# Optimization experiments

Measured on AMD Instinct MI355X. Metric: run time of the kernel, lower is better.

## Reference

```python
import jax, jax.numpy as jnp
import numpy as np


def setup_inputs() -> dict:
    key = jax.random.key(0)
    k1, k2, k3, k4 = jax.random.split(key, 4)
    B, S, D = 8, 2048, 512
    scale = 1.0 / np.sqrt(D)
    return {
        "x": jax.random.normal(k1, (B, S, D), dtype=jnp.float32),
        "WQ": jax.random.normal(k2, (D, D), dtype=jnp.float32) * scale,
        "WK": jax.random.normal(k3, (D, D), dtype=jnp.float32) * scale,
        "WV": jax.random.normal(k4, (D, D), dtype=jnp.float32) * scale,
    }


def reference(x, WQ, WK, WV):
    # x: [B, S, D]; single-head scaled dot-product self-attention
    Q = jnp.einsum("bsd,de->bse", x, WQ)
    K = jnp.einsum("bsd,de->bse", x, WK)
    V = jnp.einsum("bsd,de->bse", x, WV)
    d_k = jnp.asarray(K.shape[-1], dtype=x.dtype)
    scores = jnp.einsum("bqd,bkd->bqk", Q, K) / jnp.sqrt(d_k)  # [B,S,S]
    weights = jax.nn.softmax(scores, axis=-1)
    return jnp.einsum("bqk,bkd->bqd", weights, V)
```

## Files before the change

kernel.cpp:

```cpp
#include <hip/hip_runtime.h>
#include <cstdint>
#include <cstddef>

#define B_ 8
#define S_ 2048
#define D_ 512

typedef float f32x4 __attribute__((ext_vector_type(4)));
typedef __bf16 bf16x8 __attribute__((ext_vector_type(8)));

__device__ __forceinline__ unsigned short f2bf(float f) {
    unsigned u = __builtin_bit_cast(unsigned, f);
    u += 0x7FFFu + ((u >> 16) & 1u);
    return (unsigned short)(u >> 16);
}

template<int MT>
__global__ __launch_bounds__(256, (MT == 8) ? 2 : 3) void gemm_bt(
    const unsigned short* __restrict__ A,
    const unsigned short* __restrict__ B,
    void* __restrict__ Cv,
    unsigned short* __restrict__ Cv2,
    float* __restrict__ rs_part,
    int K, int lda, int ldb, int ldc,
    long long sA, long long sB, long long sC,
    float scale, int mode, int ntn, int nbatch)
{
    constexpr int TM = MT * 32;
    __shared__ __align__(16) unsigned short lA[TM * 32];
    __shared__ __align__(16) unsigned short lB[128 * 32];

    const int lin = blockIdx.x;
    const int bz  = lin % nbatch;
    const int t   = lin / nbatch;
    const int tn  = t % ntn;
    const int tm  = t / ntn;

    A += (long long)bz * sA;
    B += (long long)bz * sB;
    const int m0 = tm * TM;
    const int n0 = tn * 128;
    const int tid  = threadIdx.x;
    const int lane = tid & 63;
    const int wave = tid >> 6;
    const int wm = (wave & 1) * (MT * 16);
    const int wn = (wave >> 1) * 64;

    f32x4 acc[MT][4] = {};

    const int abase = wave * (MT * 512);
    const unsigned short* Ap[MT / 2];
    int aoff[MT / 2];
    #pragma unroll
    for (int j = 0; j < MT / 2; ++j) {
        const int o = abase + j * 1024 + lane * 16;
        aoff[j] = o;
        const int r = o >> 6, cp = (o & 63) >> 4;
        const int c = (cp ^ ((r >> 1) & 3)) << 3;
        Ap[j] = A + (size_t)(m0 + r) * lda + c;
    }
    const int bo0 = wave * 2048, bo1 = bo0 + 1024;
    const int ob0 = bo0 + lane * 16, ob1 = bo1 + lane * 16;
    const int rB0 = ob0 >> 6, cB0 = ((((ob0 & 63) >> 4) ^ ((rB0 >> 1) & 3)) << 3);
    const int rB1 = ob1 >> 6, cB1 = ((((ob1 & 63) >> 4) ^ ((rB1 >> 1) & 3)) << 3);
    const unsigned short* B0 = B + (size_t)(n0 + rB0) * ldb + cB0;
    const unsigned short* B1 = B + (size_t)(n0 + rB1) * ldb + cB1;

    char* lAc = (char*)lA;
    char* lBc = (char*)lB;

    const int fr  = lane & 15;
    const int g   = lane >> 4;
    const int sx  = (g ^ ((fr >> 1) & 3)) << 3;

    bf16x8 sa[MT / 2], sb0, sb1;
    #pragma unroll
    for (int j = 0; j < MT / 2; ++j)
        sa[j] = *(const bf16x8*)(Ap[j]);
    sb0 = *(const bf16x8*)(B0);
    sb1 = *(const bf16x8*)(B1);

    for (int k0 = 0; k0 < K; k0 += 32) {
        __syncthreads();
        #pragma unroll
        for (int j = 0; j < MT / 2; ++j)
            *(bf16x8*)(lAc + aoff[j]) = sa[j];
        *(bf16x8*)(lBc + ob0) = sb0;
        *(bf16x8*)(lBc + ob1) = sb1;
        __syncthreads();

        if (k0 + 32 < K) {
            #pragma unroll
            for (int j = 0; j < MT / 2; ++j)
                sa[j] = *(const bf16x8*)(Ap[j] + k0 + 32);
            sb0 = *(const bf16x8*)(B0 + k0 + 32);
            sb1 = *(const bf16x8*)(B1 + k0 + 32);
        }

        bf16x8 af[MT], bfv[4];
        #pragma unroll
        for (int mt = 0; mt < MT; ++mt)
            af[mt] = *(const bf16x8*)&lA[(wm + mt * 16 + fr) * 32 + sx];
        #pragma unroll
        for (int nt = 0; nt < 4; ++nt)
            bfv[nt] = *(const bf16x8*)&lB[(wn + nt * 16 + fr) * 32 + sx];
        #pragma unroll
        for (int mt = 0; mt < MT; ++mt)
            #pragma unroll
            for (int nt = 0; nt < 4; ++nt)
                acc[mt][nt] = __builtin_amdgcn_mfma_f32_16x16x32_bf16(
                    af[mt], bfv[nt], acc[mt][nt], 0, 0, 0);
    }

    const int rb = g << 2;

    if (mode == 1) {
        #pragma unroll
        for (int mt = 0; mt < MT; ++mt)
            #pragma unroll
            for (int nt = 0; nt < 4; ++nt)
                #pragma unroll
                for (int r = 0; r < 4; ++r)
                    acc[mt][nt][r] = __expf(acc[mt][nt][r] * scale);

        unsigned short* C = (unsigned short*)Cv + (long long)bz * sC;
        #pragma unroll
        for (int mt = 0; mt < MT; ++mt)
            #pragma unroll
            for (int nt = 0; nt < 4; ++nt) {
                const int gc = n0 + wn + nt * 16 + fr;
                #pragma unroll
                for (int r = 0; r < 4; ++r)
                    C[(size_t)(m0 + wm + mt * 16 + rb + r) * ldc + gc] =
                        f2bf(acc[mt][nt][r]);
            }

        float* rp = rs_part + (((long long)bz * S_) << 5) + tn * 2 + (wn >> 6);
        #pragma unroll
        for (int mt = 0; mt < MT; ++mt)
            #pragma unroll
            for (int r = 0; r < 4; ++r) {
                float s = acc[mt][0][r] + acc[mt][1][r] +
                          acc[mt][2][r] + acc[mt][3][r];
                s += __shfl_xor(s, 8);
                s += __shfl_xor(s, 4);
                s += __shfl_xor(s, 2);
                s += __shfl_xor(s, 1);
                if (fr == 0)
                    rp[(long long)(m0 + wm + mt * 16 + rb + r) << 5] = s;
            }
    } else if (mode == 3) {
        if (tn >= 8) {
            #pragma unroll
            for (int mt = 0; mt < MT; ++mt) {
                const int s0q = m0 + wm + mt * 16 + rb;
                const int b   = s0q >> 11;
                const int se  = s0q & (S_ - 1);
                #pragma unroll
                for (int nt = 0; nt < 4; ++nt) {
                    const int d = (n0 - 1024) + wn + nt * 16 + fr;
                    ushort4 u;
                    u.x = f2bf(acc[mt][nt][0]);
                    u.y = f2bf(acc[mt][nt][1]);
                    u.z = f2bf(acc[mt][nt][2]);
                    u.w = f2bf(acc[mt][nt][3]);
                    *(ushort4*)&Cv2[((size_t)b * D_ + d) * S_ + se] = u;
                }
            }
        } else {
            unsigned short* C = (unsigned short*)Cv;
            #pragma unroll
            for (int mt = 0; mt < MT; ++mt)
                #pragma unroll
                for (int nt = 0; nt < 4; ++nt) {
                    const int gc = n0 + wn + nt * 16 + fr;
                    #pragma unroll
                    for (int r = 0; r < 4; ++r)
                        C[(size_t)(m0 + wm + mt * 16 + rb + r) * ldc + gc] =
                            f2bf(acc[mt][nt][r]);
                }
        }
    } else {
        float* C = (float*)Cv + (long long)bz * sC;
        #pragma unroll
        for (int nt = 0; nt < 4; ++nt) {
            const int q = n0 + wn + nt * 16 + fr;
            const float* rp = rs_part + (((long long)bz * S_ + q) << 5);
            float ssum = 0.f;
            #pragma unroll
            for (int pq = 0; pq < 8; ++pq) {
                const float4 p4 = *(const float4*)(rp + 4 * pq);
                ssum += (p4.x + p4.y) + (p4.z + p4.w);
            }
            const float inv = __builtin_amdgcn_rcpf(ssum);
            #pragma unroll
            for (int mt = 0; mt < MT; ++mt) {
                const int d0 = m0 + wm + mt * 16 + rb;
                float4 o;
                o.x = acc[mt][nt][0] * inv;
                o.y = acc[mt][nt][1] * inv;
                o.z = acc[mt][nt][2] * inv;
                o.w = acc[mt][nt][3] * inv;
                *(float4*)&C[(size_t)q * ldc + d0] = o;
            }
        }
    }
}

__global__ __launch_bounds__(256) void convert_x4(const float* __restrict__ x,
                                                  unsigned short* __restrict__ xb) {
    const size_t i = ((size_t)blockIdx.x * 256 + threadIdx.x) * 4;
    const float4 f = *(const float4*)(x + i);
    ushort4 u;
    u.x = f2bf(f.x); u.y = f2bf(f.y); u.z = f2bf(f.z); u.w = f2bf(f.w);
    *(ushort4*)(xb + i) = u;
}

__global__ __launch_bounds__(256) void convert_w(const float* __restrict__ WQ,
                                                 const float* __restrict__ WK,
                                                 const float* __restrict__ WV,
                                                 unsigned short* __restrict__ WT) {
    const int o = blockIdx.x * 256 + threadIdx.x;
    const float* W = blockIdx.y == 0 ? WQ : (blockIdx.y == 1 ? WK : WV);
    const int e = o >> 9, d = o & (D_ - 1);
    WT[(size_t)blockIdx.y * D_ * D_ + o] = f2bf(W[d * D_ + e]);
}

extern "C" void kernel_launch(void* const* d_in, const int* in_sizes, int n_in,
                              void* d_out, int out_size, void* d_ws, size_t ws_size,
                              hipStream_t stream)
{
    const float* x  = (const float*)d_in[0];
    const float* WQ = (const float*)d_in[1];
    const float* WK = (const float*)d_in[2];
    const float* WV = (const float*)d_in[3];

    unsigned short* ws  = (unsigned short*)d_ws;
    const size_t NX = (size_t)B_ * S_ * D_;
    unsigned short* xb  = ws;
    unsigned short* wtb = xb + NX;
    unsigned short* qk  = wtb + 3 * D_ * D_;
    unsigned short* vtb = qk + NX * 2;
    unsigned short* sb  = vtb + NX;
    float* rsp = (float*)(sb + (size_t)B_ * S_ * S_);

    convert_x4<<<dim3((unsigned)(NX / 4 / 256)), 256, 0, stream>>>(x, xb);
    convert_w<<<dim3(D_ * D_ / 256, 3), 256, 0, stream>>>(WQ, WK, WV, wtb);

    gemm_bt<8><<<dim3((B_ * S_ / 256) * (3 * D_ / 128)), 256, 0, stream>>>(
        xb, wtb, qk, vtb, nullptr, D_, D_, D_, 2 * D_,
        0, 0, 0, 1.0f, 3,  3 * D_ / 128,  1);

    gemm_bt<8><<<dim3(B_ * (S_ / 256) * (S_ / 128)), 256, 0, stream>>>(
        qk , qk + D_ , sb, nullptr, rsp, D_, 2 * D_, 2 * D_, S_,
        (long long)S_ * 2 * D_, (long long)S_ * 2 * D_, (long long)S_ * S_,
        0.04419417382415922f, 1,  S_ / 128,  B_);

    gemm_bt<4><<<dim3(B_ * (D_ / 128) * (S_ / 128)), 256, 0, stream>>>(
        vtb, sb, d_out, nullptr, rsp, S_, S_, S_, D_,
        (long long)D_ * S_, (long long)S_ * S_, (long long)S_ * D_,
        1.0f, 0,  S_ / 128,  B_);
}
```

Baseline: 235.7 us.

## Rewrite GEMM as 8-wave 256x256 tile with direct global-to-LDS async double buffering

Replaces the 4-wave register-staged GEMM with an 8-wave kernel using 256x256 (or 128x256) tiles, K-step 64, and global_load_lds to stream tiles straight into a double-buffered swizzled LDS. The main loop is split into four phases, each with explicit vmcnt waits and barriers, so half-tile loads overlap MFMA work, and s_setprio raises priority during the MFMA bursts. The goal is to cut LDS staging through registers, raise arithmetic intensity and hide memory latency. Larger tiles give fewer blocks per GEMM, which risks lower occupancy and tail imbalance. The hand-counted vmcnt values are fragile.

```diff
diff --git a/kernel.cpp b/kernel.cpp
--- a/kernel.cpp
+++ b/kernel.cpp
@@ -15,8 +15,18 @@
     return (unsigned short)(u >> 16);
 }
 
-template<int MT>
-__global__ __launch_bounds__(256, (MT == 8) ? 2 : 3) void gemm_bt(
+__device__ __forceinline__ void gll16(const void* g, void* l) {
+    __builtin_amdgcn_global_load_lds(
+        (const __attribute__((address_space(1))) unsigned int*)g,
+        (__attribute__((address_space(3))) unsigned int*)l, 16, 0, 0);
+}
+
+#define VMCNT(n) asm volatile("s_waitcnt vmcnt(%0)" :: "i"(n) : "memory")
+#define PHASE_FENCE() do { asm volatile("" ::: "memory"); \
+                           __builtin_amdgcn_sched_barrier(0); } while (0)
+
+template<int AMT, int BNT>
+__global__ __launch_bounds__(512, 2) void gemm8(
     const unsigned short* __restrict__ A,
     const unsigned short* __restrict__ B,
     void* __restrict__ Cv,
@@ -26,139 +36,187 @@
     long long sA, long long sB, long long sC,
     float scale, int mode, int ntn, int nbatch)
 {
-    constexpr int TM = MT * 32;
-    __shared__ __align__(16) unsigned short lA[TM * 32];
-    __shared__ __align__(16) unsigned short lB[128 * 32];
+    constexpr int BM     = 64 * AMT;
+    constexpr int BN     = 128 * BNT;
+    constexpr int ABYTES = BM * 128;
+    constexpr int BBYTES = BN * 128;
+    constexpr int AH     = ABYTES / 2;
+    constexpr int BH     = BBYTES / 2;
+    constexpr int AGL    = AMT / 2;
+    constexpr int BGL    = BNT;
+    constexpr int BUFB   = ABYTES + BBYTES;
+    __shared__ __align__(16) char lds[2 * BUFB];
 
     const int lin = blockIdx.x;
     const int bz  = lin % nbatch;
-    const int t   = lin / nbatch;
-    const int tn  = t % ntn;
-    const int tm  = t / ntn;
-
+    const int tq  = lin / nbatch;
+    const int tn  = tq % ntn;
+    const int tm  = tq / ntn;
     A += (long long)bz * sA;
     B += (long long)bz * sB;
-    const int m0 = tm * TM;
-    const int n0 = tn * 128;
+    const int m0   = tm * BM;
+    const int n0   = tn * BN;
     const int tid  = threadIdx.x;
     const int lane = tid & 63;
-    const int wave = tid >> 6;
-    const int wm = (wave & 1) * (MT * 16);
-    const int wn = (wave >> 1) * 64;
-
-    f32x4 acc[MT][4] = {};
-
-    const int abase = wave * (MT * 512);
-    const unsigned short* Ap[MT / 2];
-    int aoff[MT / 2];
+    const int w    = tid >> 6;
+    const int g2   = w >> 2;
+    const int nb   = w & 3;
+
+    const int lrow = lane >> 3;
+    const int swz  = ((lane & 7) ^ lrow) << 3;
+    const unsigned short* gA[2][AGL];
+    const unsigned short* gB[2][BGL];
     #pragma unroll
-    for (int j = 0; j < MT / 2; ++j) {
-        const int o = abase + j * 1024 + lane * 16;
-        aoff[j] = o;
-        const int r = o >> 6, cp = (o & 63) >> 4;
-        const int c = (cp ^ ((r >> 1) & 3)) << 3;
-        Ap[j] = A + (size_t)(m0 + r) * lda + c;
+    for (int h = 0; h < 2; ++h) {
+        #pragma unroll
+        for (int i = 0; i < AGL; ++i)
+            gA[h][i] = A + (size_t)(m0 + h * (BM / 2) + (w * AGL + i) * 8 + lrow) * lda + swz;
+        #pragma unroll
+        for (int i = 0; i < BGL; ++i)
+            gB[h][i] = B + (size_t)(n0 + h * (BN / 2) + (w * BGL + i) * 8 + lrow) * ldb + swz;
     }
-    const int bo0 = wave * 2048, bo1 = bo0 + 1024;
-    const int ob0 = bo0 + lane * 16, ob1 = bo1 + lane * 16;
-    const int rB0 = ob0 >> 6, cB0 = ((((ob0 & 63) >> 4) ^ ((rB0 >> 1) & 3)) << 3);
-    const int rB1 = ob1 >> 6, cB1 = ((((ob1 & 63) >> 4) ^ ((rB1 >> 1) & 3)) << 3);
-    const unsigned short* B0 = B + (size_t)(n0 + rB0) * ldb + cB0;
-    const unsigned short* B1 = B + (size_t)(n0 + rB1) * ldb + cB1;
-
-    char* lAc = (char*)lA;
-    char* lBc = (char*)lB;
-
-    const int fr  = lane & 15;
-    const int g   = lane >> 4;
-    const int sx  = (g ^ ((fr >> 1) & 3)) << 3;
-
-    bf16x8 sa[MT / 2], sb0, sb1;
+    auto stA = [&](int bs, int h, int kof) {
+        #pragma unroll
+        for (int i = 0; i < AGL; ++i)
+            gll16(gA[h][i] + kof, lds + bs * BUFB + h * AH + (w * AGL + i) * 1024);
+    };
+    auto stB = [&](int bs, int h, int kof) {
+        #pragma unroll
+        for (int i = 0; i < BGL; ++i)
+            gll16(gB[h][i] + kof, lds + bs * BUFB + ABYTES + h * BH + (w * BGL + i) * 1024);
+    };
+
+    const int fr = lane & 15;
+    const int gq = lane >> 4;
+    const int c0 = (gq ^ (fr & 7)) << 4;
+    int aoff[AMT], boff[BNT];
     #pragma unroll
-    for (int j = 0; j < MT / 2; ++j)
-        sa[j] = *(const bf16x8*)(Ap[j]);
-    sb0 = *(const bf16x8*)(B0);
-    sb1 = *(const bf16x8*)(B1);
-
-    for (int k0 = 0; k0 < K; k0 += 32) {
-        __syncthreads();
-        #pragma unroll
-        for (int j = 0; j < MT / 2; ++j)
-            *(bf16x8*)(lAc + aoff[j]) = sa[j];
-        *(bf16x8*)(lBc + ob0) = sb0;
-        *(bf16x8*)(lBc + ob1) = sb1;
-        __syncthreads();
-
-        if (k0 + 32 < K) {
-            #pragma unroll
-            for (int j = 0; j < MT / 2; ++j)
-                sa[j] = *(const bf16x8*)(Ap[j] + k0 + 32);
-            sb0 = *(const bf16x8*)(B0 + k0 + 32);
-            sb1 = *(const bf16x8*)(B1 + k0 + 32);
-        }
-
-        bf16x8 af[MT], bfv[4];
-        #pragma unroll
-        for (int mt = 0; mt < MT; ++mt)
-            af[mt] = *(const bf16x8*)&lA[(wm + mt * 16 + fr) * 32 + sx];
-        #pragma unroll
-        for (int nt = 0; nt < 4; ++nt)
-            bfv[nt] = *(const bf16x8*)&lB[(wn + nt * 16 + fr) * 32 + sx];
-        #pragma unroll
-        for (int mt = 0; mt < MT; ++mt)
-            #pragma unroll
-            for (int nt = 0; nt < 4; ++nt)
-                acc[mt][nt] = __builtin_amdgcn_mfma_f32_16x16x32_bf16(
-                    af[mt], bfv[nt], acc[mt][nt], 0, 0, 0);
+    for (int ml = 0; ml < AMT; ++ml)
+        aoff[ml] = (g2 * (16 * AMT) + ml * 16 + fr) * 128 + c0;
+    #pragma unroll
+    for (int nl = 0; nl < BNT; ++nl)
+        boff[nl] = (nb * (16 * BNT) + nl * 16 + fr) * 128 + c0;
+
+    bf16x8 af[2 * AMT], bLO[2 * BNT], bHI[2 * BNT];
+    f32x4 acc[2 * AMT][2 * BNT] = {};
+
+    auto ldA = [&](const char* Ab, int mh) {
+        #pragma unroll
+        for (int ml = 0; ml < AMT; ++ml)
+            #pragma unroll
+            for (int kk = 0; kk < 2; ++kk)
+                af[ml * 2 + kk] = *(const bf16x8*)(Ab + mh * AH + (aoff[ml] ^ (kk << 6)));
+    };
+    auto ldB = [&](const char* Bb, int nh, bf16x8* bf) {
+        #pragma unroll
+        for (int nl = 0; nl < BNT; ++nl)
+            #pragma unroll
+            for (int kk = 0; kk < 2; ++kk)
+                bf[nl * 2 + kk] = *(const bf16x8*)(Bb + nh * BH + (boff[nl] ^ (kk << 6)));
+    };
+    auto mma = [&](int mh, int nh, const bf16x8* bf) {
+        __builtin_amdgcn_s_setprio(1);
+        #pragma unroll
+        for (int ml = 0; ml < AMT; ++ml)
+            #pragma unroll
+            for (int nl = 0; nl < BNT; ++nl)
+                #pragma unroll
+                for (int kk = 0; kk < 2; ++kk)
+                    acc[mh * AMT + ml][nh * BNT + nl] =
+                        __builtin_amdgcn_mfma_f32_16x16x32_bf16(
+                            af[ml * 2 + kk], bf[nl * 2 + kk],
+                            acc[mh * AMT + ml][nh * BNT + nl], 0, 0, 0);
+        __builtin_amdgcn_s_setprio(0);
+    };
+
+    stA(0, 0, 0);  stB(0, 0, 0);
+    stA(0, 1, 0);  stB(0, 1, 0);
+    stA(1, 0, 64); stB(1, 0, 64);
+
+    const int NT = K >> 6;
+    for (int tt = 0; tt < NT; ++tt) {
+        const int bs = tt & 1;
+        const char* Ab = lds + bs * BUFB;
+        const char* Bb = Ab + ABYTES;
+        const bool last = (tt == NT - 1);
+
+        if (!last) stA(bs ^ 1, 1, (tt + 1) << 6);
+        if (last) { VMCNT(AGL + BGL); } else { VMCNT(6); }
+        __builtin_amdgcn_s_barrier();
+        PHASE_FENCE();
+        ldA(Ab, 0); ldB(Bb, 0, bLO);
+        mma(0, 0, bLO);
+
+        if (!last) stB(bs ^ 1, 1, (tt + 1) << 6);
+        if (last) { VMCNT(0); } else { VMCNT(6); }
+        __builtin_amdgcn_s_barrier();
+        PHASE_FENCE();
+        ldB(Bb, 1, bHI);
+        mma(0, 1, bHI);
+
+        if (tt + 2 < NT) stA(bs, 0, (tt + 2) << 6);
+        VMCNT(6);
+        __builtin_amdgcn_s_barrier();
+        PHASE_FENCE();
+        ldA(Ab, 1);
+        mma(1, 0, bLO);
+
+        if (tt + 2 < NT) stB(bs, 0, (tt + 2) << 6);
+        VMCNT(6);
+        __builtin_amdgcn_s_barrier();
+        PHASE_FENCE();
+        mma(1, 1, bHI);
     }
 
-    const int rb = g << 2;
+    const int rb4 = gq << 2;
+#define AB_(mt) ((((mt) / AMT) * (BM / 2)) + g2 * (16 * AMT) + ((mt) % AMT) * 16)
+#define BB_(nt) ((((nt) / BNT) * (BN / 2)) + nb * (16 * BNT) + ((nt) % BNT) * 16)
 
     if (mode == 1) {
         #pragma unroll
-        for (int mt = 0; mt < MT; ++mt)
-            #pragma unroll
-            for (int nt = 0; nt < 4; ++nt)
+        for (int mt = 0; mt < 2 * AMT; ++mt)
+            #pragma unroll
+            for (int nt = 0; nt < 2 * BNT; ++nt)
                 #pragma unroll
                 for (int r = 0; r < 4; ++r)
                     acc[mt][nt][r] = __expf(acc[mt][nt][r] * scale);
 
         unsigned short* C = (unsigned short*)Cv + (long long)bz * sC;
         #pragma unroll
-        for (int mt = 0; mt < MT; ++mt)
-            #pragma unroll
-            for (int nt = 0; nt < 4; ++nt) {
-                const int gc = n0 + wn + nt * 16 + fr;
+        for (int mt = 0; mt < 2 * AMT; ++mt)
+            #pragma unroll
+            for (int nt = 0; nt < 2 * BNT; ++nt) {
+                const int gc = n0 + BB_(nt) + fr;
                 #pragma unroll
                 for (int r = 0; r < 4; ++r)
-                    C[(size_t)(m0 + wm + mt * 16 + rb + r) * ldc + gc] =
-                        f2bf(acc[mt][nt][r]);
-            }
-
-        float* rp = rs_part + (((long long)bz * S_) << 5) + tn * 2 + (wn >> 6);
-        #pragma unroll
-        for (int mt = 0; mt < MT; ++mt)
+                    C[(size_t)(m0 + AB_(mt) + rb4 + r) * ldc + gc] = f2bf(acc[mt][nt][r]);
+            }
+
+        float* rp = rs_part + (((long long)bz * S_) << 5) + tn * 4 + nb;
+        #pragma unroll
+        for (int mt = 0; mt < 2 * AMT; ++mt)
             #pragma unroll
             for (int r = 0; r < 4; ++r) {
-                float s = acc[mt][0][r] + acc[mt][1][r] +
-                          acc[mt][2][r] + acc[mt][3][r];
+                float s = 0.f;
+                #pragma unroll
+                for (int nt = 0; nt < 2 * BNT; ++nt) s += acc[mt][nt][r];
                 s += __shfl_xor(s, 8);
                 s += __shfl_xor(s, 4);
                 s += __shfl_xor(s, 2);
                 s += __shfl_xor(s, 1);
                 if (fr == 0)
-                    rp[(long long)(m0 + wm + mt * 16 + rb + r) << 5] = s;
+                    rp[(long long)(m0 + AB_(mt) + rb4 + r) << 5] = s;
             }
     } else if (mode == 3) {
-        if (tn >= 8) {
-            #pragma unroll
-            for (int mt = 0; mt < MT; ++mt) {
-                const int s0q = m0 + wm + mt * 16 + rb;
+        if (tn >= 4) {
+            #pragma unroll
+            for (int mt = 0; mt < 2 * AMT; ++mt) {
+                const int s0q = m0 + AB_(mt) + rb4;
                 const int b   = s0q >> 11;
                 const int se  = s0q & (S_ - 1);
                 #pragma unroll
-                for (int nt = 0; nt < 4; ++nt) {
-                    const int d = (n0 - 1024) + wn + nt * 16 + fr;
+                for (int nt = 0; nt < 2 * BNT; ++nt) {
+                    const int d = (n0 - 2 * D_) + BB_(nt) + fr;
                     ushort4 u;
                     u.x = f2bf(acc[mt][nt][0]);
                     u.y = f2bf(acc[mt][nt][1]);
@@ -170,21 +228,20 @@
         } else {
             unsigned short* C = (unsigned short*)Cv;
             #pragma unroll
-            for (int mt = 0; mt < MT; ++mt)
-                #pragma unroll
-                for (int nt = 0; nt < 4; ++nt) {
-                    const int gc = n0 + wn + nt * 16 + fr;
+            for (int mt = 0; mt < 2 * AMT; ++mt)
+                #pragma unroll
+                for (int nt = 0; nt < 2 * BNT; ++nt) {
+                    const int gc = n0 + BB_(nt) + fr;
                     #pragma unroll
                     for (int r = 0; r < 4; ++r)
-                        C[(size_t)(m0 + wm + mt * 16 + rb + r) * ldc + gc] =
-                            f2bf(acc[mt][nt][r]);
+                        C[(size_t)(m0 + AB_(mt) + rb4 + r) * ldc + gc] = f2bf(acc[mt][nt][r]);
                 }
         }
     } else {
         float* C = (float*)Cv + (long long)bz * sC;
         #pragma unroll
-        for (int nt = 0; nt < 4; ++nt) {
-            const int q = n0 + wn + nt * 16 + fr;
+        for (int nt = 0; nt < 2 * BNT; ++nt) {
+            const int q = n0 + BB_(nt) + fr;
             const float* rp = rs_part + (((long long)bz * S_ + q) << 5);
             float ssum = 0.f;
             #pragma unroll
@@ -194,8 +251,8 @@
             }
             const float inv = __builtin_amdgcn_rcpf(ssum);
             #pragma unroll
-            for (int mt = 0; mt < MT; ++mt) {
-                const int d0 = m0 + wm + mt * 16 + rb;
+            for (int mt = 0; mt < 2 * AMT; ++mt) {
+                const int d0 = m0 + AB_(mt) + rb4;
                 float4 o;
                 o.x = acc[mt][nt][0] * inv;
                 o.y = acc[mt][nt][1] * inv;
@@ -205,6 +262,8 @@
             }
         }
     }
+#undef AB_
+#undef BB_
 }
 
 __global__ __launch_bounds__(256) void convert_x4(const float* __restrict__ x,
@@ -247,17 +306,17 @@
     convert_x4<<<dim3((unsigned)(NX / 4 / 256)), 256, 0, stream>>>(x, xb);
     convert_w<<<dim3(D_ * D_ / 256, 3), 256, 0, stream>>>(WQ, WK, WV, wtb);
 
-    gemm_bt<8><<<dim3((B_ * S_ / 256) * (3 * D_ / 128)), 256, 0, stream>>>(
+    gemm8<4, 2><<<dim3(384), 512, 0, stream>>>(
         xb, wtb, qk, vtb, nullptr, D_, D_, D_, 2 * D_,
-        0, 0, 0, 1.0f, 3,  3 * D_ / 128,  1);
-
-    gemm_bt<8><<<dim3(B_ * (S_ / 256) * (S_ / 128)), 256, 0, stream>>>(
+        0, 0, 0, 1.0f, 3,  6,  1);
+
+    gemm8<4, 2><<<dim3(512), 512, 0, stream>>>(
         qk , qk + D_ , sb, nullptr, rsp, D_, 2 * D_, 2 * D_, S_,
         (long long)S_ * 2 * D_, (long long)S_ * 2 * D_, (long long)S_ * S_,
-        0.04419417382415922f, 1,  S_ / 128,  B_);
-
-    gemm_bt<4><<<dim3(B_ * (D_ / 128) * (S_ / 128)), 256, 0, stream>>>(
+        0.04419417382415922f, 1,  8,  8);
+
+    gemm8<2, 2><<<dim3(256), 512, 0, stream>>>(
         vtb, sb, d_out, nullptr, rsp, S_, S_, S_, D_,
         (long long)D_ * S_, (long long)S_ * S_, (long long)S_ * D_,
-        1.0f, 0,  S_ / 128,  B_);
-}
+        1.0f, 0,  8,  8);
+}
```

Measured after the change: 228.2 us. 3.2% less time.

## Load GEMM tiles directly into LDS and unify on 128x128 tiles

Applied to the files above, without the earlier changes.

Replaces the register-staged global-to-LDS copy with global_load_lds direct-to-shared loads and collapses the templated kernel into a single 128x128 tile variant for all three GEMMs. This drops the VGPR staging and the separate LDS write step, and changes the grid sizes for the QKV and score GEMMs, which previously used 256-row tiles. The next tile is now issued only after the compute and a second barrier, with no double buffering. This can expose load latency and gives less reuse per block for the larger GEMMs.

```diff
diff --git a/kernel.cpp b/kernel.cpp
--- a/kernel.cpp
+++ b/kernel.cpp
@@ -15,8 +15,13 @@
     return (unsigned short)(u >> 16);
 }
 
-template<int MT>
-__global__ __launch_bounds__(256, (MT == 8) ? 2 : 3) void gemm_bt(
+__device__ __forceinline__ void gll16(const void* g, void* l) {
+    __builtin_amdgcn_global_load_lds(
+        (const __attribute__((address_space(1))) unsigned int*)g,
+        (__attribute__((address_space(3))) unsigned int*)l, 16, 0, 0);
+}
+
+__global__ __launch_bounds__(256) void gemm97(
     const unsigned short* __restrict__ A,
     const unsigned short* __restrict__ B,
     void* __restrict__ Cv,
@@ -26,97 +31,86 @@
     long long sA, long long sB, long long sC,
     float scale, int mode, int ntn, int nbatch)
 {
-    constexpr int TM = MT * 32;
-    __shared__ __align__(16) unsigned short lA[TM * 32];
+    __shared__ __align__(16) unsigned short lA[128 * 32];
     __shared__ __align__(16) unsigned short lB[128 * 32];
 
     const int lin = blockIdx.x;
     const int bz  = lin % nbatch;
-    const int t   = lin / nbatch;
-    const int tn  = t % ntn;
-    const int tm  = t / ntn;
-
+    const int tq  = lin / nbatch;
+    const int tn  = tq % ntn;
+    const int tm  = tq / ntn;
     A += (long long)bz * sA;
     B += (long long)bz * sB;
-    const int m0 = tm * TM;
-    const int n0 = tn * 128;
+    const int m0   = tm * 128;
+    const int n0   = tn * 128;
     const int tid  = threadIdx.x;
     const int lane = tid & 63;
-    const int wave = tid >> 6;
-    const int wm = (wave & 1) * (MT * 16);
-    const int wn = (wave >> 1) * 64;
-
-    f32x4 acc[MT][4] = {};
-
-    const int abase = wave * (MT * 512);
-    const unsigned short* Ap[MT / 2];
-    int aoff[MT / 2];
+    const int w    = tid >> 6;
+    const int wm   = (w & 1) * 64;
+    const int wn   = (w >> 1) * 64;
+
+    const unsigned short* gA[2];
+    const unsigned short* gB[2];
+    int lo[2];
     #pragma unroll
-    for (int j = 0; j < MT / 2; ++j) {
-        const int o = abase + j * 1024 + lane * 16;
-        aoff[j] = o;
-        const int r = o >> 6, cp = (o & 63) >> 4;
-        const int c = (cp ^ ((r >> 1) & 3)) << 3;
-        Ap[j] = A + (size_t)(m0 + r) * lda + c;
-    }
-    const int bo0 = wave * 2048, bo1 = bo0 + 1024;
-    const int ob0 = bo0 + lane * 16, ob1 = bo1 + lane * 16;
-    const int rB0 = ob0 >> 6, cB0 = ((((ob0 & 63) >> 4) ^ ((rB0 >> 1) & 3)) << 3);
-    const int rB1 = ob1 >> 6, cB1 = ((((ob1 & 63) >> 4) ^ ((rB1 >> 1) & 3)) << 3);
-    const unsigned short* B0 = B + (size_t)(n0 + rB0) * ldb + cB0;
-    const unsigned short* B1 = B + (size_t)(n0 + rB1) * ldb + cB1;
-
-    char* lAc = (char*)lA;
-    char* lBc = (char*)lB;
-
-    const int fr  = lane & 15;
-    const int g   = lane >> 4;
-    const int sx  = (g ^ ((fr >> 1) & 3)) << 3;
-
-    bf16x8 sa[MT / 2], sb0, sb1;
+    for (int j = 0; j < 2; ++j) {
+        const int o  = tid * 16 + j * 4096;
+        lo[j] = o;
+        const int r  = o >> 6, cp = (o & 63) >> 4;
+        const int c  = (cp ^ ((r >> 1) & 3)) << 3;
+        gA[j] = A + (size_t)(m0 + r) * lda + c;
+        gB[j] = B + (size_t)(n0 + r) * ldb + c;
+    }
+    char* lac = (char*)lA;
+    char* lbc = (char*)lB;
+    auto stage = [&](int k0) {
+        gll16(gA[0] + k0, lac + lo[0]);
+        gll16(gA[1] + k0, lac + lo[1]);
+        gll16(gB[0] + k0, lbc + lo[0]);
+        gll16(gB[1] + k0, lbc + lo[1]);
+    };
+
+    const int fr = lane & 15;
+    const int gq = lane >> 4;
+    int aoff[4], boff[4];
     #pragma unroll
-    for (int j = 0; j < MT / 2; ++j)
-        sa[j] = *(const bf16x8*)(Ap[j]);
-    sb0 = *(const bf16x8*)(B0);
-    sb1 = *(const bf16x8*)(B1);
-
+    for (int mt = 0; mt < 4; ++mt) {
+        const int r = wm + mt * 16 + fr;
+        aoff[mt] = r * 64 + ((gq ^ ((r >> 1) & 3)) << 4);
+    }
+    #pragma unroll
+    for (int nt = 0; nt < 4; ++nt) {
+        const int r = wn + nt * 16 + fr;
+        boff[nt] = r * 64 + ((gq ^ ((r >> 1) & 3)) << 4);
+    }
+
+    f32x4 acc[4][4] = {};
+
+    stage(0);
     for (int k0 = 0; k0 < K; k0 += 32) {
         __syncthreads();
-        #pragma unroll
-        for (int j = 0; j < MT / 2; ++j)
-            *(bf16x8*)(lAc + aoff[j]) = sa[j];
-        *(bf16x8*)(lBc + ob0) = sb0;
-        *(bf16x8*)(lBc + ob1) = sb1;
-        __syncthreads();
-
-        if (k0 + 32 < K) {
-            #pragma unroll
-            for (int j = 0; j < MT / 2; ++j)
-                sa[j] = *(const bf16x8*)(Ap[j] + k0 + 32);
-            sb0 = *(const bf16x8*)(B0 + k0 + 32);
-            sb1 = *(const bf16x8*)(B1 + k0 + 32);
-        }
-
-        bf16x8 af[MT], bfv[4];
-        #pragma unroll
-        for (int mt = 0; mt < MT; ++mt)
-            af[mt] = *(const bf16x8*)&lA[(wm + mt * 16 + fr) * 32 + sx];
+        bf16x8 af[4], bf[4];
+        #pragma unroll
+        for (int mt = 0; mt < 4; ++mt)
+            af[mt] = *(const bf16x8*)(lac + aoff[mt]);
         #pragma unroll
         for (int nt = 0; nt < 4; ++nt)
-            bfv[nt] = *(const bf16x8*)&lB[(wn + nt * 16 + fr) * 32 + sx];
-        #pragma unroll
-        for (int mt = 0; mt < MT; ++mt)
+            bf[nt] = *(const bf16x8*)(lbc + boff[nt]);
+        #pragma unroll
+        for (int mt = 0; mt < 4; ++mt)
             #pragma unroll
             for (int nt = 0; nt < 4; ++nt)
                 acc[mt][nt] = __builtin_amdgcn_mfma_f32_16x16x32_bf16(
-                    af[mt], bfv[nt], acc[mt][nt], 0, 0, 0);
-    }
-
-    const int rb = g << 2;
+                    af[mt], bf[nt], acc[mt][nt], 0, 0, 0);
+        __syncthreads();
+        if (k0 + 32 < K) stage(k0 + 32);
+    }
+
+    const int rb = gq << 2;
 
     if (mode == 1) {
         #pragma unroll
-        for (int mt = 0; mt < MT; ++mt)
+        for (int mt = 0; mt < 4; ++mt)
             #pragma unroll
             for (int nt = 0; nt < 4; ++nt)
                 #pragma unroll
@@ -125,7 +119,7 @@
 
         unsigned short* C = (unsigned short*)Cv + (long long)bz * sC;
         #pragma unroll
-        for (int mt = 0; mt < MT; ++mt)
+        for (int mt = 0; mt < 4; ++mt)
             #pragma unroll
             for (int nt = 0; nt < 4; ++nt) {
                 const int gc = n0 + wn + nt * 16 + fr;
@@ -137,7 +131,7 @@
 
         float* rp = rs_part + (((long long)bz * S_) << 5) + tn * 2 + (wn >> 6);
         #pragma unroll
-        for (int mt = 0; mt < MT; ++mt)
+        for (int mt = 0; mt < 4; ++mt)
             #pragma unroll
             for (int r = 0; r < 4; ++r) {
                 float s = acc[mt][0][r] + acc[mt][1][r] +
@@ -152,7 +146,7 @@
     } else if (mode == 3) {
         if (tn >= 8) {
             #pragma unroll
-            for (int mt = 0; mt < MT; ++mt) {
+            for (int mt = 0; mt < 4; ++mt) {
                 const int s0q = m0 + wm + mt * 16 + rb;
                 const int b   = s0q >> 11;
                 const int se  = s0q & (S_ - 1);
@@ -170,7 +164,7 @@
         } else {
             unsigned short* C = (unsigned short*)Cv;
             #pragma unroll
-            for (int mt = 0; mt < MT; ++mt)
+            for (int mt = 0; mt < 4; ++mt)
                 #pragma unroll
                 for (int nt = 0; nt < 4; ++nt) {
                     const int gc = n0 + wn + nt * 16 + fr;
@@ -194,7 +188,7 @@
             }
             const float inv = __builtin_amdgcn_rcpf(ssum);
             #pragma unroll
-            for (int mt = 0; mt < MT; ++mt) {
+            for (int mt = 0; mt < 4; ++mt) {
                 const int d0 = m0 + wm + mt * 16 + rb;
                 float4 o;
                 o.x = acc[mt][nt][0] * inv;
@@ -247,17 +241,17 @@
     convert_x4<<<dim3((unsigned)(NX / 4 / 256)), 256, 0, stream>>>(x, xb);
     convert_w<<<dim3(D_ * D_ / 256, 3), 256, 0, stream>>>(WQ, WK, WV, wtb);
 
-    gemm_bt<8><<<dim3((B_ * S_ / 256) * (3 * D_ / 128)), 256, 0, stream>>>(
+    gemm97<<<dim3(1536), 256, 0, stream>>>(
         xb, wtb, qk, vtb, nullptr, D_, D_, D_, 2 * D_,
-        0, 0, 0, 1.0f, 3,  3 * D_ / 128,  1);
-
-    gemm_bt<8><<<dim3(B_ * (S_ / 256) * (S_ / 128)), 256, 0, stream>>>(
+        0, 0, 0, 1.0f, 3,  12,  1);
+
+    gemm97<<<dim3(2048), 256, 0, stream>>>(
         qk , qk + D_ , sb, nullptr, rsp, D_, 2 * D_, 2 * D_, S_,
         (long long)S_ * 2 * D_, (long long)S_ * 2 * D_, (long long)S_ * S_,
-        0.04419417382415922f, 1,  S_ / 128,  B_);
-
-    gemm_bt<4><<<dim3(B_ * (D_ / 128) * (S_ / 128)), 256, 0, stream>>>(
+        0.04419417382415922f, 1,  16,  8);
+
+    gemm97<<<dim3(512), 256, 0, stream>>>(
         vtb, sb, d_out, nullptr, rsp, S_, S_, S_, D_,
         (long long)D_ * S_, (long long)S_ * S_, (long long)S_ * D_,
-        1.0f, 0,  S_ / 128,  B_);
-}
+        1.0f, 0,  16,  8);
+}
```

New measurement: 273.3 us. 16.0% more time.
